# Optimization experiments

Measured on AMD Instinct MI355X. Metric: run time of the kernel, lower is better.

## Reference

```python
import math
import jax, jax.numpy as jnp
import numpy as np

B, C, N = 32, 1024, 4096  # batch, feature channels, points


def setup_inputs() -> dict:
    key = jax.random.key(0)
    kx, kw = jax.random.split(key)
    x = jax.random.normal(kx, (B, 3, N), dtype=jnp.float32)
    W = jax.random.normal(kw, (C, 3), dtype=jnp.float32) * 0.1  # pointwise feature extractor (stand-in for `model`)
    return {"x": x, "W": W}


def my_entropy(x):
    # Faithful to torch my_entropy, with the normalization done per-row
    # (torch code omits keepdim, which only type-checks when B==N; per-row
    # normalization is the clearly intended math).
    eps = 1e-6
    n = x.shape[-1]
    x = x + eps
    x = x / jnp.sum(x, axis=-1, keepdims=True)
    ent = -jnp.sum(x * jnp.log2(x), axis=-1) / math.log2(n)
    return ent  # [B]


def reference(x, W):
    b, _, n = x.shape
    # model(x)[1]: pointwise features  [B, C, N]
    x_f = jnp.einsum('cd,bdn->bcn', W, x)
    # critical point index per channel (torch.max(..., dim=-1)[1])  [B, C]
    imp = jnp.argmax(x_f, axis=-1)
    # batched bincount(minlength=N) via one flat segment_sum (replaces the
    # per-batch python loop of tiny bincount kernels)
    flat_ids = (imp + jnp.arange(b, dtype=imp.dtype)[:, None] * n).reshape(-1)
    counts = jax.ops.segment_sum(
        jnp.ones(flat_ids.shape, jnp.float32), flat_ids, num_segments=b * n
    ).reshape(b, n)  # imp3, float like torch's zeros-buffer  [B, N]
    # imp2: ascending argsort of per-point counts (stored as float in torch)
    imp2 = jnp.argsort(counts, axis=-1).astype(jnp.float32)  # [B, N]
    ent = my_entropy(counts)  # [B]
    # torch forward returns importance_ppc (= x); we also return the computed
    # imp3/imp2/ent so the histogram+argsort+entropy work is not dead code.
    return (x, counts, imp2, ent)
```

## Files before the change

kernel.cpp:

```cpp
#include <hip/hip_runtime.h>
#include <math.h>

#define BB 32
#define CC 1024
#define NN 4096
#define NCH 16
#define CHK 256

typedef unsigned long long u64;

__device__ __forceinline__ u64 enc_key(float v, int gidx) {
    unsigned u = __float_as_uint(v);
    unsigned mono = (u & 0x80000000u) ? ~u : (u | 0x80000000u);
    return ((u64)mono << 12) | (unsigned)(4095 - gidx);
}

__global__ __launch_bounds__(256) void k1_argmax_partial(
    const float* __restrict__ x, const float* __restrict__ W,
    float* __restrict__ out_x, u64* __restrict__ pkeys) {
    const int bid = blockIdx.x;
    const int b = bid >> 4, k = bid & 15;
    const int tid = threadIdx.x;

    if (tid < 192) {
        int d = tid >> 6;
        int off = (tid & 63) << 2;
        const size_t p = (size_t)(b * 3 + d) * NN + k * CHK + off;
        *(float4*)(out_x + p) = *(const float4*)(x + p);
    }

    float w0[4], w1[4], w2[4];
    #pragma unroll
    for (int q = 0; q < 4; ++q) {
        int c = q * 256 + tid;
        w0[q] = W[c * 3 + 0];
        w1[q] = W[c * 3 + 1];
        w2[q] = W[c * 3 + 2];
    }

    const float* xb = x + (size_t)b * 3 * NN + k * CHK;
    float best[4] = {-INFINITY, -INFINITY, -INFINITY, -INFINITY};
    int gn[4] = {0, 0, 0, 0};

    #pragma unroll 4
    for (int n = 0; n < CHK; n += 4) {
        float4 a0 = *(const float4*)(xb + n);
        float4 a1 = *(const float4*)(xb + NN + n);
        float4 a2 = *(const float4*)(xb + 2 * NN + n);
        #pragma unroll
        for (int q = 0; q < 4; ++q) {
            float v0 = fmaf(w2[q], a2.x, fmaf(w1[q], a1.x, w0[q] * a0.x));
            float v1 = fmaf(w2[q], a2.y, fmaf(w1[q], a1.y, w0[q] * a0.y));
            float v2 = fmaf(w2[q], a2.z, fmaf(w1[q], a1.z, w0[q] * a0.z));
            float v3 = fmaf(w2[q], a2.w, fmaf(w1[q], a1.w, w0[q] * a0.w));
            float gm = fmaxf(fmaxf(v0, v1), fmaxf(v2, v3));
            if (gm > best[q]) { best[q] = gm; gn[q] = n; }
        }
    }

    #pragma unroll
    for (int q = 0; q < 4; ++q) {
        int n = gn[q];
        float4 a0 = *(const float4*)(xb + n);
        float4 a1 = *(const float4*)(xb + NN + n);
        float4 a2 = *(const float4*)(xb + 2 * NN + n);
        float v0 = fmaf(w2[q], a2.x, fmaf(w1[q], a1.x, w0[q] * a0.x));
        float v1 = fmaf(w2[q], a2.y, fmaf(w1[q], a1.y, w0[q] * a0.y));
        float v2 = fmaf(w2[q], a2.z, fmaf(w1[q], a1.z, w0[q] * a0.z));
        int j = (v0 == best[q]) ? 0 : (v1 == best[q]) ? 1 : (v2 == best[q]) ? 2 : 3;
        pkeys[(size_t)(b * NCH + k) * CC + q * 256 + tid] =
            enc_key(best[q], k * CHK + n + j);
    }
}

__global__ __launch_bounds__(1024) void k2_row(
    const u64* __restrict__ pkeys, float* __restrict__ counts,
    int* __restrict__ cumP, float* __restrict__ ent) {
    __shared__ int cnt[NN];
    __shared__ int H[NCH * (CC + 1)];
    __shared__ int sc[1024];
    __shared__ float red[1024];
    __shared__ int exv[CC + 1];

    const int b = blockIdx.x;
    const int tid = threadIdx.x;
    const int wv = tid >> 6, lane = tid & 63;

    #pragma unroll
    for (int i = 0; i < 4; ++i) cnt[tid + i * 1024] = 0;
    for (int i = tid; i < NCH * (CC + 1); i += 1024) H[i] = 0;
    __syncthreads();

    {
        u64 bestk = 0;
        const u64* pk = pkeys + (size_t)b * NCH * CC + tid;
        #pragma unroll
        for (int k = 0; k < NCH; ++k) {
            u64 key = pk[k * CC];
            bestk = (key > bestk) ? key : bestk;
        }
        int idx = 4095 - (int)(bestk & 0xFFFu);
        atomicAdd(&cnt[idx], 1);
    }
    __syncthreads();

    {
        float4 cf;
        cf.x = (float)cnt[4 * tid + 0];
        cf.y = (float)cnt[4 * tid + 1];
        cf.z = (float)cnt[4 * tid + 2];
        cf.w = (float)cnt[4 * tid + 3];
        *(float4*)(counts + (size_t)b * NN + 4 * tid) = cf;

        int h0 = 0, h1 = 0;
        #pragma unroll
        for (int r = 0; r < 4; ++r) {
            int ci = cnt[wv * CHK + r * 64 + lane];
            u64 m0 = __ballot(ci == 0);
            u64 m1 = __ballot(ci == 1);
            if (lane == 0) { h0 += (int)__popcll(m0); h1 += (int)__popcll(m1); }
            if (ci > 1) atomicAdd(&H[wv * (CC + 1) + ci], 1);
        }
        if (lane == 0) {
            H[wv * (CC + 1) + 0] = h0;
            H[wv * (CC + 1) + 1] = h1;
        }
    }
    __syncthreads();

    int g_v = 0;
    #pragma unroll
    for (int w = 0; w < NCH; ++w) g_v += H[w * (CC + 1) + tid];
    sc[tid] = g_v;
    __syncthreads();
    for (int off = 1; off < 1024; off <<= 1) {
        int v = sc[tid];
        int add = (tid >= off) ? sc[tid - off] : 0;
        __syncthreads();
        sc[tid] = v + add;
        __syncthreads();
    }
    exv[tid] = (tid > 0) ? sc[tid - 1] : 0;
    if (tid == 0) exv[CC] = sc[1023];
    __syncthreads();

    {
        int run = exv[tid];
        int* cp = cumP + (size_t)b * NCH * (CC + 1) + tid;
        #pragma unroll
        for (int k = 0; k < NCH; ++k) {
            cp[k * (CC + 1)] = run;
            run += H[k * (CC + 1) + tid];
        }
        if (tid == 0) {
            int run2 = exv[CC];
            int* cp2 = cumP + (size_t)b * NCH * (CC + 1) + CC;
            for (int k = 0; k < NCH; ++k) {
                cp2[k * (CC + 1)] = run2;
                run2 += H[k * (CC + 1) + CC];
            }
        }
    }

    const float S = 1024.0f + 4096.0f * 1e-6f;
    float e = 0.f;
    if (g_v) {
        float p = ((float)tid + 1e-6f) / S;
        e = (float)g_v * p * log2f(p);
    }
    if (tid == 0) {
        int g1024 = 0;
        #pragma unroll
        for (int w = 0; w < NCH; ++w) g1024 += H[w * (CC + 1) + CC];
        if (g1024) {
            float p = (1024.0f + 1e-6f) / S;
            e += (float)g1024 * p * log2f(p);
        }
    }
    red[tid] = e;
    __syncthreads();
    for (int off = 512; off > 0; off >>= 1) {
        if (tid < off) red[tid] += red[tid + off];
        __syncthreads();
    }
    if (tid == 0) ent[b] = -red[0] / 12.0f;
}

__global__ __launch_bounds__(256) void k3_place(
    const float* __restrict__ counts, const int* __restrict__ cumP,
    float* __restrict__ imp2) {
    __shared__ int cvs[CHK];
    const int bid = blockIdx.x;
    const int b = bid >> 4, k = bid & 15;
    const int tid = threadIdx.x;
    const int n = k * CHK + tid;

    int ci = (int)(counts[(size_t)b * NN + n] + 0.5f);
    cvs[tid] = ci;
    __syncthreads();

    int rank = 0;
    #pragma unroll 8
    for (int j = 0; j < CHK - 1; ++j)
        rank += (j < tid && cvs[j] == ci) ? 1 : 0;

    int pos = cumP[(size_t)(b * NCH + k) * (CC + 1) + ci] + rank;
    imp2[(size_t)b * NN + pos] = (float)n;
}

extern "C" void kernel_launch(void* const* d_in, const int* in_sizes, int n_in,
                              void* d_out, int out_size, void* d_ws, size_t ws_size,
                              hipStream_t stream) {
    const float* x = (const float*)d_in[0];
    const float* W = (const float*)d_in[1];
    float* out    = (float*)d_out;
    float* out_x  = out;
    float* counts = out + (size_t)BB * 3 * NN;
    float* imp2   = counts + (size_t)BB * NN;
    float* ent    = imp2 + (size_t)BB * NN;

    u64* pkeys = (u64*)d_ws;
    int* cumP  = (int*)(pkeys + (size_t)BB * NCH * CC);

    k1_argmax_partial<<<BB * NCH, 256, 0, stream>>>(x, W, out_x, pkeys);
    k2_row<<<BB, 1024, 0, stream>>>(pkeys, counts, cumP, ent);
    k3_place<<<BB * NCH, 256, 0, stream>>>(counts, cumP, imp2);
}
```

Baseline: 88.75 us.

## Fuse argsort placement into row kernel with wave-level scans

Result: faster. 79.77 us (-10.1%).

```diff
diff --git a/kernel.cpp b/kernel.cpp
--- a/kernel.cpp
+++ b/kernel.cpp
@@ -73,14 +73,14 @@
     }
 }
 
-__global__ __launch_bounds__(1024) void k2_row(
+__global__ __launch_bounds__(1024) void k2_row_all(
     const u64* __restrict__ pkeys, float* __restrict__ counts,
-    int* __restrict__ cumP, float* __restrict__ ent) {
-    __shared__ int cnt[NN];
-    __shared__ int H[NCH * (CC + 1)];
-    __shared__ int sc[1024];
-    __shared__ float red[1024];
-    __shared__ int exv[CC + 1];
+    float* __restrict__ imp2, float* __restrict__ ent) {
+    __shared__ int   cnt[NN];
+    __shared__ int   H[NCH * (CC + 1)];
+    __shared__ int   exvs[CC + 1];
+    __shared__ int   wsum[16];
+    __shared__ float esum[16];
 
     const int b = blockIdx.x;
     const int tid = threadIdx.x;
@@ -88,7 +88,9 @@
 
     #pragma unroll
     for (int i = 0; i < 4; ++i) cnt[tid + i * 1024] = 0;
-    for (int i = tid; i < NCH * (CC + 1); i += 1024) H[i] = 0;
+    #pragma unroll
+    for (int i = 0; i < 16; ++i) H[tid + i * 1024] = 0;
+    if (tid < NCH * (CC + 1) - 16 * 1024) H[16 * 1024 + tid] = 0;
     __syncthreads();
 
     {
@@ -128,84 +130,96 @@
     }
     __syncthreads();
 
-    int g_v = 0;
-    #pragma unroll
-    for (int w = 0; w < NCH; ++w) g_v += H[w * (CC + 1) + tid];
-    sc[tid] = g_v;
-    __syncthreads();
-    for (int off = 1; off < 1024; off <<= 1) {
-        int v = sc[tid];
-        int add = (tid >= off) ? sc[tid - off] : 0;
-        __syncthreads();
-        sc[tid] = v + add;
-        __syncthreads();
-    }
-    exv[tid] = (tid > 0) ? sc[tid - 1] : 0;
-    if (tid == 0) exv[CC] = sc[1023];
-    __syncthreads();
-
-    {
-        int run = exv[tid];
-        int* cp = cumP + (size_t)b * NCH * (CC + 1) + tid;
-        #pragma unroll
-        for (int k = 0; k < NCH; ++k) {
-            cp[k * (CC + 1)] = run;
-            run += H[k * (CC + 1) + tid];
-        }
+    int g_v, run1024 = 0;
+    {
+        int run = 0;
+        #pragma unroll
+        for (int w = 0; w < NCH; ++w) {
+            int t = H[w * (CC + 1) + tid];
+            H[w * (CC + 1) + tid] = run;
+            run += t;
+        }
+        g_v = run;
         if (tid == 0) {
-            int run2 = exv[CC];
-            int* cp2 = cumP + (size_t)b * NCH * (CC + 1) + CC;
-            for (int k = 0; k < NCH; ++k) {
-                cp2[k * (CC + 1)] = run2;
-                run2 += H[k * (CC + 1) + CC];
+            int run2 = 0;
+            #pragma unroll
+            for (int w = 0; w < NCH; ++w) {
+                int t = H[w * (CC + 1) + CC];
+                H[w * (CC + 1) + CC] = run2;
+                run2 += t;
             }
-        }
-    }
-
+            run1024 = run2;
+        }
+    }
     const float S = 1024.0f + 4096.0f * 1e-6f;
     float e = 0.f;
     if (g_v) {
         float p = ((float)tid + 1e-6f) / S;
         e = (float)g_v * p * log2f(p);
     }
-    if (tid == 0) {
-        int g1024 = 0;
-        #pragma unroll
-        for (int w = 0; w < NCH; ++w) g1024 += H[w * (CC + 1) + CC];
-        if (g1024) {
-            float p = (1024.0f + 1e-6f) / S;
-            e += (float)g1024 * p * log2f(p);
-        }
-    }
-    red[tid] = e;
-    __syncthreads();
-    for (int off = 512; off > 0; off >>= 1) {
-        if (tid < off) red[tid] += red[tid + off];
-        __syncthreads();
-    }
-    if (tid == 0) ent[b] = -red[0] / 12.0f;
-}
-
-__global__ __launch_bounds__(256) void k3_place(
-    const float* __restrict__ counts, const int* __restrict__ cumP,
-    float* __restrict__ imp2) {
-    __shared__ int cvs[CHK];
-    const int bid = blockIdx.x;
-    const int b = bid >> 4, k = bid & 15;
-    const int tid = threadIdx.x;
-    const int n = k * CHK + tid;
-
-    int ci = (int)(counts[(size_t)b * NN + n] + 0.5f);
-    cvs[tid] = ci;
-    __syncthreads();
-
-    int rank = 0;
-    #pragma unroll 8
-    for (int j = 0; j < CHK - 1; ++j)
-        rank += (j < tid && cvs[j] == ci) ? 1 : 0;
-
-    int pos = cumP[(size_t)(b * NCH + k) * (CC + 1) + ci] + rank;
-    imp2[(size_t)b * NN + pos] = (float)n;
+    if (tid == 0 && run1024) {
+        float p = (1024.0f + 1e-6f) / S;
+        e += (float)run1024 * p * log2f(p);
+    }
+    int incl = g_v;
+    #pragma unroll
+    for (int d = 1; d < 64; d <<= 1) {
+        int t = __shfl_up(incl, d, 64);
+        if (lane >= d) incl += t;
+    }
+    float er = e;
+    #pragma unroll
+    for (int d = 32; d > 0; d >>= 1)
+        er += __shfl_down(er, d, 64);
+    if (lane == 63) wsum[wv] = incl;
+    if (lane == 0)  esum[wv] = er;
+    __syncthreads();
+
+    if (wv == 0) {
+        int v = (lane < 16) ? wsum[lane] : 0;
+        int inc2 = v;
+        #pragma unroll
+        for (int d = 1; d < 16; d <<= 1) {
+            int t = __shfl_up(inc2, d, 64);
+            if (lane >= d) inc2 += t;
+        }
+        if (lane < 16) wsum[lane] = inc2 - v;
+    } else if (wv == 1) {
+        float v = (lane < 16) ? esum[lane] : 0.f;
+        #pragma unroll
+        for (int d = 8; d > 0; d >>= 1)
+            v += __shfl_down(v, d, 64);
+        if (lane == 0) ent[b] = -v / 12.0f;
+    }
+    __syncthreads();
+
+    exvs[tid] = incl - g_v + wsum[wv];
+    if (tid == 0) exvs[CC] = NN - run1024;
+    __syncthreads();
+
+    {
+        const u64 ltmask = (1ull << lane) - 1ull;
+        int* curw = &H[wv * (CC + 1)];
+        float* orow = imp2 + (size_t)b * NN;
+        for (int r = 0; r < 4; ++r) {
+            const int n = wv * CHK + r * 64 + lane;
+            const int ci = cnt[n];
+            u64 eq = 0, todo = ~0ull;
+            while (true) {
+                int src = (int)__builtin_ctzll(todo);
+                int v0 = __shfl(ci, src, 64);
+                u64 m = __ballot(ci == v0);
+                if (ci == v0) eq = m;
+                todo &= ~m;
+                if (todo == 0ull) break;
+            }
+            int rank = (int)__popcll(eq & ltmask);
+            int c0 = curw[ci];
+            orow[c0 + exvs[ci] + rank] = (float)n;
+            if ((eq >> lane) == 1ull)
+                curw[ci] = c0 + (int)__popcll(eq);
+        }
+    }
 }
 
 extern "C" void kernel_launch(void* const* d_in, const int* in_sizes, int n_in,
@@ -220,9 +234,7 @@
     float* ent    = imp2 + (size_t)BB * NN;
 
     u64* pkeys = (u64*)d_ws;
-    int* cumP  = (int*)(pkeys + (size_t)BB * NCH * CC);
 
     k1_argmax_partial<<<BB * NCH, 256, 0, stream>>>(x, W, out_x, pkeys);
-    k2_row<<<BB, 1024, 0, stream>>>(pkeys, counts, cumP, ent);
-    k3_place<<<BB * NCH, 256, 0, stream>>>(counts, cumP, imp2);
-}
+    k2_row_all<<<BB, 1024, 0, stream>>>(pkeys, counts, imp2, ent);
+}
```
